# Performance work log

Measured on AMD Instinct MI355X. Metric: run time of the kernel, lower is better.

The kernel has to match this reference:

```python
import jax, jax.numpy as jnp
import numpy as np

N, IN_DIM, OUT_DIM = 8192, 512, 512
ALPHA = 0.2  # leaky relu negative slope
NEG_BIG = -9e15

def _xavier(key, shape, gain=1.414):
    fan_in, fan_out = shape[0], shape[1]
    bound = gain * np.sqrt(6.0 / (fan_in + fan_out))
    return jax.random.uniform(key, shape, jnp.float32, -bound, bound)

def setup_inputs() -> dict:
    key = jax.random.key(0)
    k1, k2, k3, k4 = jax.random.split(key, 4)
    h = jax.random.normal(k1, (N, IN_DIM), jnp.float32)
    adj = jax.random.randint(k2, (N, N), 0, 2, jnp.int32)
    W = _xavier(k3, (IN_DIM, OUT_DIM))
    a = _xavier(k4, (2 * OUT_DIM, 1))
    return {"h": h, "adj": adj, "W": W, "a": a}

def reference(h, adj, W, a):
    Wh = h @ W                              # [N, out]
    # e_ij = leakyrelu(a1 . Wh_i + a2 . Wh_j) without the O(N^2*2d) concat
    a1 = a[:OUT_DIM, 0]                     # [out]
    a2 = a[OUT_DIM:, 0]                     # [out]
    f1 = Wh @ a1                            # [N]
    f2 = Wh @ a2                            # [N]
    e = jax.nn.leaky_relu(f1[:, None] + f2[None, :], negative_slope=ALPHA)
    e = jnp.where(adj > 0, e, NEG_BIG)
    attention = jax.nn.softmax(e, axis=1)   # dropout is identity in eval mode
    h_prime = attention @ Wh                # [N, out]
    return jax.nn.elu(h_prime)              # concat=True branch
```

## Files before the change

### kernel.cpp

```cpp
#include <hip/hip_runtime.h>
#include <stdint.h>

#define NN   8192
#define DIN  512
#define DOUT 512
#define ALPHA 0.2f

typedef float          floatx4  __attribute__((ext_vector_type(4)));
typedef float          floatx2  __attribute__((ext_vector_type(2)));
typedef short          shortx8  __attribute__((ext_vector_type(8)));
typedef unsigned short ushortx4 __attribute__((ext_vector_type(4)));
typedef int            intx2    __attribute__((ext_vector_type(2)));
typedef int            intx4    __attribute__((ext_vector_type(4)));
typedef unsigned       uintx2   __attribute__((ext_vector_type(2)));

__device__ inline unsigned short f2bf(float x) {
    union { float f; unsigned u; } v; v.f = x;
    return (unsigned short)((v.u + 0x7FFFu + ((v.u >> 16) & 1u)) >> 16);
}
__device__ inline unsigned encf(float x) {
    union { float f; unsigned u; } v; v.f = x;
    return (v.u & 0x80000000u) ? ~v.u : (v.u | 0x80000000u);
}
__device__ inline float decf(unsigned e) {
    union { float f; unsigned u; } v;
    v.u = (e & 0x80000000u) ? (e & 0x7FFFFFFFu) : ~e;
    return v.f;
}
__device__ inline float lrelu(float x) { return fmaxf(x, ALPHA * x); }

__global__ __launch_bounds__(256) void transpose_w(const float* __restrict__ W,
                                                   unsigned short* __restrict__ WT) {
    __shared__ float tile[32][33];
    const int t = threadIdx.x;
    const int x = t & 31, y = t >> 5;
    const int tr = (blockIdx.x >> 4) * 32, tc = (blockIdx.x & 15) * 32;
#pragma unroll
    for (int i = 0; i < 4; i++) {
        int r = y + i * 8;
        tile[r][x] = W[(size_t)(tr + r) * DOUT + tc + x];
    }
    __syncthreads();
#pragma unroll
    for (int i = 0; i < 4; i++) {
        int r = y + i * 8;
        WT[(size_t)(tc + r) * DIN + tr + x] = f2bf(tile[x][r]);
    }
}

__global__ __launch_bounds__(256) void gemm_wh(
    const float* __restrict__ h, const unsigned short* __restrict__ WT,
    const float* __restrict__ a, unsigned short* __restrict__ WhTt,
    float* __restrict__ f1, float* __restrict__ f2, unsigned* __restrict__ Menc)
{
    __shared__ float f1s[4][16], f2s[4][16];
    const int t = threadIdx.x;
    const int w = t >> 6, lane = t & 63, l15 = lane & 15, q = lane >> 4;
    const int r0 = blockIdx.x * 16;
    const int wc0 = w * 128;

    floatx4 acc[8];
    const floatx4 z4 = {0.f, 0.f, 0.f, 0.f};
#pragma unroll
    for (int j = 0; j < 8; j++) acc[j] = z4;

    const float* hp = &h[(size_t)(r0 + l15) * DIN + q * 8];
    const unsigned short* bp = &WT[(size_t)(wc0 + l15) * DIN + q * 8];

    floatx4 hA[2][2];
    shortx8 bB[2][8];
    hA[0][0] = *(const floatx4*)hp;
    hA[0][1] = *(const floatx4*)(hp + 4);
#pragma unroll
    for (int nt = 0; nt < 8; nt++)
        bB[0][nt] = *(const shortx8*)(bp + (size_t)nt * 16 * DIN);

#pragma unroll 2
    for (int it = 0; it < 16; ++it) {
        const int c = it & 1, n = c ^ 1;
        const int kn = ((it + 1) & 15) * 32;
        hA[n][0] = *(const floatx4*)(hp + kn);
        hA[n][1] = *(const floatx4*)(hp + kn + 4);
#pragma unroll
        for (int nt = 0; nt < 8; nt++)
            bB[n][nt] = *(const shortx8*)(bp + (size_t)nt * 16 * DIN + kn);

        shortx8 af;
#pragma unroll
        for (int j = 0; j < 8; j++)
            af[j] = (short)f2bf(hA[c][j >> 2][j & 3]);
#pragma unroll
        for (int nt = 0; nt < 8; nt++)
            acc[nt] = __builtin_amdgcn_mfma_f32_16x16x32_bf16(af, bB[c][nt], acc[nt], 0, 0, 0);
    }

    float a1v[8], a2v[8];
#pragma unroll
    for (int nt = 0; nt < 8; nt++) {
        int col = wc0 + nt * 16 + l15;
        a1v[nt] = a[col];
        a2v[nt] = a[DOUT + col];
    }
    {
        const int kk0 = r0 + q * 4;
        const int tile_k = kk0 >> 5;
        const int qq = (kk0 >> 3) & 3;
        const int j0 = kk0 & 7;
#pragma unroll
        for (int nt = 0; nt < 8; nt++) {
            const int tile_n = w * 8 + nt;
            ushortx4 pk;
#pragma unroll
            for (int reg = 0; reg < 4; reg++) pk[reg] = f2bf(acc[nt][reg]);
            *(ushortx4*)&WhTt[(((size_t)tile_k * 32 + tile_n) << 9) + qq * 128 + l15 * 8 + j0] = pk;
        }
    }
    float s1a[4], s2a[4];
#pragma unroll
    for (int reg = 0; reg < 4; reg++) {
        float s1 = 0.f, s2 = 0.f;
#pragma unroll
        for (int nt = 0; nt < 8; nt++) {
            s1 += acc[nt][reg] * a1v[nt];
            s2 += acc[nt][reg] * a2v[nt];
        }
        s1 += __shfl_xor(s1, 1, 64); s2 += __shfl_xor(s2, 1, 64);
        s1 += __shfl_xor(s1, 2, 64); s2 += __shfl_xor(s2, 2, 64);
        s1 += __shfl_xor(s1, 4, 64); s2 += __shfl_xor(s2, 4, 64);
        s1 += __shfl_xor(s1, 8, 64); s2 += __shfl_xor(s2, 8, 64);
        s1a[reg] = s1; s2a[reg] = s2;
    }
    if (l15 == 0) {
#pragma unroll
        for (int reg = 0; reg < 4; reg++) {
            f1s[w][q * 4 + reg] = s1a[reg];
            f2s[w][q * 4 + reg] = s2a[reg];
        }
    }
    __syncthreads();
    if (t < 16) {
        float v1 = f1s[0][t] + f1s[1][t] + f1s[2][t] + f1s[3][t];
        float v2 = f2s[0][t] + f2s[1][t] + f2s[2][t] + f2s[3][t];
        f1[r0 + t] = v1;
        f2[r0 + t] = v2;
        float mx = v2;
        mx = fmaxf(mx, __shfl_xor(mx, 1, 64));
        mx = fmaxf(mx, __shfl_xor(mx, 2, 64));
        mx = fmaxf(mx, __shfl_xor(mx, 4, 64));
        mx = fmaxf(mx, __shfl_xor(mx, 8, 64));
        if (t == 0) atomicMax(Menc, encf(mx));
    }
}

__global__ __launch_bounds__(1024, 4) void gat_agg(
    const int* __restrict__ adj, const unsigned short* __restrict__ WhTt,
    const float* __restrict__ f1, const float* __restrict__ f2,
    const unsigned* __restrict__ Menc, float* __restrict__ P,
    float* __restrict__ D)
{
    __shared__ __align__(16) unsigned short pbuf[2][4][128 * 40];
    __shared__ float f2s[2048];
    __shared__ float lsp[8][128];

    const int t = threadIdx.x;
    const int w = t >> 6, lane = t & 63, l15 = lane & 15, q = lane >> 4;
    const int prow = t >> 3, pk = t & 7;

    const int kq = blockIdx.x & 3;
    const int rgid = blockIdx.x >> 2;
    const int r0 = rgid * 128;
    const int k0 = kq * 2048;
    const int it0 = ((blockIdx.x >> 3) * 4) & 63;

    *(floatx2*)&f2s[t * 2] = *(const floatx2*)&f2[k0 + t * 2];

    const float M = decf(*Menc);
    const float f1v = f1[r0 + prow];
    const float mi = lrelu(f1v + M);

    floatx4 acc[8][2];
    const floatx4 z4 = {0.f, 0.f, 0.f, 0.f};
#pragma unroll
    for (int i = 0; i < 8; i++)
#pragma unroll
        for (int j = 0; j < 2; j++) acc[i][j] = z4;
    float ls = 0.f;

    const unsigned short* bpp = WhTt
        + (((size_t)(kq * 64) * 32 + w * 2) << 9) + lane * 8;
    const int* arp = adj + (size_t)(r0 + prow) * NN + k0 + pk * 4;

    intx4   adjr[4];
    shortx8 breg[2][2];

    __syncthreads();

#pragma unroll
    for (int j = 0; j < 4; j++)
        adjr[j] = __builtin_nontemporal_load((const intx4*)(arp + ((it0 + j) & 63) * 32));
    breg[0][0] = *(const shortx8*)(bpp + (size_t)it0 * 16384);
    breg[0][1] = *(const shortx8*)(bpp + (size_t)it0 * 16384 + 512);

#pragma unroll 1
    for (int g = 0; g < 16; ++g) {
        const int gb = g & 1;

#pragma unroll
        for (int j = 0; j < 4; j++) {
            const int px = (g * 4 + j + it0) & 63;
            const floatx4 ff = *(const floatx4*)&f2s[px * 32 + pk * 4];
            const intx4   ad = adjr[j];
            float p0 = __expf(lrelu(f1v + ff[0]) - mi);
            float p1 = __expf(lrelu(f1v + ff[1]) - mi);
            float p2 = __expf(lrelu(f1v + ff[2]) - mi);
            float p3 = __expf(lrelu(f1v + ff[3]) - mi);
            p0 = (ad[0] > 0) ? p0 : 0.f;
            p1 = (ad[1] > 0) ? p1 : 0.f;
            p2 = (ad[2] > 0) ? p2 : 0.f;
            p3 = (ad[3] > 0) ? p3 : 0.f;
            ls += (p0 + p1) + (p2 + p3);
            uintx2 dd;
            dd[0] = __builtin_amdgcn_perm(__float_as_uint(p1), __float_as_uint(p0), 0x07060302u);
            dd[1] = __builtin_amdgcn_perm(__float_as_uint(p3), __float_as_uint(p2), 0x07060302u);
            *(uintx2*)&pbuf[gb][j][prow * 40 + pk * 4] = dd;
        }

        {
            const int gn = (g + 1) & 15;
#pragma unroll
            for (int j = 0; j < 4; j++)
                adjr[j] = __builtin_nontemporal_load(
                    (const intx4*)(arp + ((gn * 4 + j + it0) & 63) * 32));
        }

        asm volatile("s_waitcnt lgkmcnt(0)" ::: "memory");
        __builtin_amdgcn_s_barrier();

#pragma unroll
        for (int j = 0; j < 4; j++) {
            const int c = (g * 4 + j) & 1, n = c ^ 1;
            const int pxn = (g * 4 + j + 1 + it0) & 63;
            breg[n][0] = *(const shortx8*)(bpp + (size_t)pxn * 16384);
            breg[n][1] = *(const shortx8*)(bpp + (size_t)pxn * 16384 + 512);

            __builtin_amdgcn_s_setprio(1);
#pragma unroll
            for (int rg = 0; rg < 8; rg++) {
                const shortx8 af = *(const shortx8*)&pbuf[gb][j][(rg * 16 + l15) * 40 + q * 8];
                acc[rg][0] = __builtin_amdgcn_mfma_f32_16x16x32_bf16(af, breg[c][0], acc[rg][0], 0, 0, 0);
                acc[rg][1] = __builtin_amdgcn_mfma_f32_16x16x32_bf16(af, breg[c][1], acc[rg][1], 0, 0, 0);
            }
            __builtin_amdgcn_s_setprio(0);
        }
    }

    __syncthreads();
    lsp[pk][prow] = ls;
    __syncthreads();
    if (t < 128) {
        float s = 0.f;
#pragma unroll
        for (int kc = 0; kc < 8; kc++) s += lsp[kc][t];
        D[kq * NN + r0 + t] = s;
    }

    float* Pq = P + (size_t)kq * ((size_t)NN * DOUT) + (size_t)r0 * DOUT;
#pragma unroll
    for (int rg = 0; rg < 8; rg++)
#pragma unroll
        for (int nt = 0; nt < 2; nt++) {
            const int col = w * 32 + nt * 16 + l15;
#pragma unroll
            for (int reg = 0; reg < 4; reg++) {
                const int row = rg * 16 + q * 4 + reg;
                Pq[(size_t)row * DOUT + col] = acc[rg][nt][reg];
            }
        }
}

__global__ __launch_bounds__(1024) void gat_fin(
    const float* __restrict__ P, const float* __restrict__ D,
    float* __restrict__ out)
{
    const int t = threadIdx.x;
    const int r0 = blockIdx.x * 32;
    const int rr = t >> 7;
    const int c4 = (t & 127) * 4;
    const size_t Q = (size_t)NN * DOUT;
#pragma unroll
    for (int j = 0; j < 4; j++) {
        const int row = r0 + j * 8 + rr;
        const float den = ((D[row] + D[NN + row]) + (D[2 * NN + row] + D[3 * NN + row]));
        const float li = 1.f / den;
        const size_t off = (size_t)row * DOUT + c4;
        floatx4 v0 = *(const floatx4*)(P + off);
        floatx4 v1 = *(const floatx4*)(P + Q + off);
        floatx4 v2 = *(const floatx4*)(P + 2 * Q + off);
        floatx4 v3 = *(const floatx4*)(P + 3 * Q + off);
        floatx4 s;
#pragma unroll
        for (int i = 0; i < 4; i++) {
            float x = ((v0[i] + v1[i]) + (v2[i] + v3[i])) * li;
            s[i] = (x > 0.f) ? x : (__expf(x) - 1.f);
        }
        __builtin_nontemporal_store(s, (floatx4*)(out + off));
    }
}

extern "C" void kernel_launch(void* const* d_in, const int* in_sizes, int n_in,
                              void* d_out, int out_size, void* d_ws, size_t ws_size,
                              hipStream_t stream) {
    const float* h   = (const float*)d_in[0];
    const int*   adj = (const int*)d_in[1];
    const float* W   = (const float*)d_in[2];
    const float* a   = (const float*)d_in[3];
    float* out = (float*)d_out;

    char* ws = (char*)d_ws;
    unsigned short* WT    = (unsigned short*)ws;
    unsigned short* WhTt  = (unsigned short*)(ws + 524288);
    float*          f1    = (float*)(ws + 8912896);
    float*          f2    = (float*)(ws + 8945664);
    unsigned*       Menc  = (unsigned*)(ws + 8978432);
    float*          D     = (float*)(ws + 9437184);
    float*          P     = (float*)(ws + 16777216);

    hipMemsetAsync(Menc, 0, 4, stream);
    transpose_w<<<256, 256, 0, stream>>>(W, WT);
    gemm_wh<<<512, 256, 0, stream>>>(h, WT, a, WhTt, f1, f2, Menc);
    gat_agg<<<256, 1024, 0, stream>>>(adj, WhTt, f1, f2, Menc, P, D);
    gat_fin<<<256, 1024, 0, stream>>>(P, D, out);
}
```

Measured before the change: 432.8 us.

## Software-pipeline softmax P-tile computation with MFMA over double-buffered LDS

Restructures the aggregation loop so the exp/mask computation for the next group of tiles is interleaved with the MFMA work on the current group, writing into the other LDS buffer. A prologue fills the first buffer, and there is now one barrier per group, after the MFMAs, instead of one between the two phases. The f2 staging array in shared memory is removed and f2 is read straight from global memory (likely cache hits). The intent is to hide exp and adjacency-load latency behind matrix-core work. The cost is higher register pressure and more global loads of f2.

```diff
diff --git a/kernel.cpp b/kernel.cpp
--- a/kernel.cpp
+++ b/kernel.cpp
@@ -159,7 +159,6 @@
     float* __restrict__ D)
 {
     __shared__ __align__(16) unsigned short pbuf[2][4][128 * 40];
-    __shared__ float f2s[2048];
     __shared__ float lsp[8][128];
 
     const int t = threadIdx.x;
@@ -172,8 +171,6 @@
     const int k0 = kq * 2048;
     const int it0 = ((blockIdx.x >> 3) * 4) & 63;
 
-    *(floatx2*)&f2s[t * 2] = *(const floatx2*)&f2[k0 + t * 2];
-
     const float M = decf(*Menc);
     const float f1v = f1[r0 + prow];
     const float mi = lrelu(f1v + M);
@@ -189,59 +186,74 @@
     const unsigned short* bpp = WhTt
         + (((size_t)(kq * 64) * 32 + w * 2) << 9) + lane * 8;
     const int* arp = adj + (size_t)(r0 + prow) * NN + k0 + pk * 4;
+    const float* fpq = f2 + k0 + pk * 4;
 
     intx4   adjr[4];
     shortx8 breg[2][2];
 
-    __syncthreads();
-
 #pragma unroll
     for (int j = 0; j < 4; j++)
         adjr[j] = __builtin_nontemporal_load((const intx4*)(arp + ((it0 + j) & 63) * 32));
+#pragma unroll
+    for (int j = 0; j < 4; j++) {
+        const int px = (it0 + j) & 63;
+        const floatx4 ff = *(const floatx4*)(fpq + px * 32);
+        const intx4   ad = adjr[j];
+        float p0 = __expf(lrelu(f1v + ff[0]) - mi);
+        float p1 = __expf(lrelu(f1v + ff[1]) - mi);
+        float p2 = __expf(lrelu(f1v + ff[2]) - mi);
+        float p3 = __expf(lrelu(f1v + ff[3]) - mi);
+        p0 = (ad[0] > 0) ? p0 : 0.f;
+        p1 = (ad[1] > 0) ? p1 : 0.f;
+        p2 = (ad[2] > 0) ? p2 : 0.f;
+        p3 = (ad[3] > 0) ? p3 : 0.f;
+        ls += (p0 + p1) + (p2 + p3);
+        uintx2 dd;
+        dd[0] = __builtin_amdgcn_perm(__float_as_uint(p1), __float_as_uint(p0), 0x07060302u);
+        dd[1] = __builtin_amdgcn_perm(__float_as_uint(p3), __float_as_uint(p2), 0x07060302u);
+        *(uintx2*)&pbuf[0][j][prow * 40 + pk * 4] = dd;
+    }
+#pragma unroll
+    for (int j = 0; j < 4; j++)
+        adjr[j] = __builtin_nontemporal_load((const intx4*)(arp + ((4 + j + it0) & 63) * 32));
     breg[0][0] = *(const shortx8*)(bpp + (size_t)it0 * 16384);
     breg[0][1] = *(const shortx8*)(bpp + (size_t)it0 * 16384 + 512);
+    asm volatile("s_waitcnt lgkmcnt(0)" ::: "memory");
+    __builtin_amdgcn_s_barrier();
 
 #pragma unroll 1
     for (int g = 0; g < 16; ++g) {
         const int gb = g & 1;
-
 #pragma unroll
         for (int j = 0; j < 4; j++) {
-            const int px = (g * 4 + j + it0) & 63;
-            const floatx4 ff = *(const floatx4*)&f2s[px * 32 + pk * 4];
-            const intx4   ad = adjr[j];
-            float p0 = __expf(lrelu(f1v + ff[0]) - mi);
-            float p1 = __expf(lrelu(f1v + ff[1]) - mi);
-            float p2 = __expf(lrelu(f1v + ff[2]) - mi);
-            float p3 = __expf(lrelu(f1v + ff[3]) - mi);
-            p0 = (ad[0] > 0) ? p0 : 0.f;
-            p1 = (ad[1] > 0) ? p1 : 0.f;
-            p2 = (ad[2] > 0) ? p2 : 0.f;
-            p3 = (ad[3] > 0) ? p3 : 0.f;
-            ls += (p0 + p1) + (p2 + p3);
-            uintx2 dd;
-            dd[0] = __builtin_amdgcn_perm(__float_as_uint(p1), __float_as_uint(p0), 0x07060302u);
-            dd[1] = __builtin_amdgcn_perm(__float_as_uint(p3), __float_as_uint(p2), 0x07060302u);
-            *(uintx2*)&pbuf[gb][j][prow * 40 + pk * 4] = dd;
-        }
-
-        {
-            const int gn = (g + 1) & 15;
-#pragma unroll
-            for (int j = 0; j < 4; j++)
-                adjr[j] = __builtin_nontemporal_load(
-                    (const intx4*)(arp + ((gn * 4 + j + it0) & 63) * 32));
-        }
-
-        asm volatile("s_waitcnt lgkmcnt(0)" ::: "memory");
-        __builtin_amdgcn_s_barrier();
-
-#pragma unroll
-        for (int j = 0; j < 4; j++) {
-            const int c = (g * 4 + j) & 1, n = c ^ 1;
-            const int pxn = (g * 4 + j + 1 + it0) & 63;
+            const int ft = g * 4 + j;
+            const int c = ft & 1, n = c ^ 1;
+            const int pxn = (ft + 1 + it0) & 63;
+
             breg[n][0] = *(const shortx8*)(bpp + (size_t)pxn * 16384);
             breg[n][1] = *(const shortx8*)(bpp + (size_t)pxn * 16384 + 512);
+
+            if (g < 15) {
+                const int px = ((g + 1) * 4 + j + it0) & 63;
+                const floatx4 ff = *(const floatx4*)(fpq + px * 32);
+                const intx4   ad = adjr[j];
+                float p0 = __expf(lrelu(f1v + ff[0]) - mi);
+                float p1 = __expf(lrelu(f1v + ff[1]) - mi);
+                float p2 = __expf(lrelu(f1v + ff[2]) - mi);
+                float p3 = __expf(lrelu(f1v + ff[3]) - mi);
+                p0 = (ad[0] > 0) ? p0 : 0.f;
+                p1 = (ad[1] > 0) ? p1 : 0.f;
+                p2 = (ad[2] > 0) ? p2 : 0.f;
+                p3 = (ad[3] > 0) ? p3 : 0.f;
+                ls += (p0 + p1) + (p2 + p3);
+                uintx2 dd;
+                dd[0] = __builtin_amdgcn_perm(__float_as_uint(p1), __float_as_uint(p0), 0x07060302u);
+                dd[1] = __builtin_amdgcn_perm(__float_as_uint(p3), __float_as_uint(p2), 0x07060302u);
+                *(uintx2*)&pbuf[gb ^ 1][j][prow * 40 + pk * 4] = dd;
+                if (g < 14)
+                    adjr[j] = __builtin_nontemporal_load(
+                        (const intx4*)(arp + (((g + 2) * 4 + j + it0) & 63) * 32));
+            }
 
             __builtin_amdgcn_s_setprio(1);
 #pragma unroll
@@ -252,6 +264,8 @@
             }
             __builtin_amdgcn_s_setprio(0);
         }
+        asm volatile("s_waitcnt lgkmcnt(0)" ::: "memory");
+        __builtin_amdgcn_s_barrier();
     }
 
     __syncthreads();
```

After: 500.3 us. 15.6% more time.

## Store partial accumulators in fragment-native layout and remap in finalize kernel

Applied to the files above, without the earlier changes.

The attention kernel now writes each MFMA accumulator fragment as one contiguous 16-byte vector store in a fragment-ordered layout, replacing scattered strided scalar stores. The finalize kernel reads the four partials in that same layout with coalesced vector loads, takes per-row inverse denominators from shared memory, and does the layout-to-row-major transposition while storing the output. The aim is to make the large partial-sum writes coalesced. In exchange, the final output stores become scalar and partly strided.

```diff
diff --git a/kernel.cpp b/kernel.cpp
--- a/kernel.cpp
+++ b/kernel.cpp
@@ -264,46 +264,54 @@
         D[kq * NN + r0 + t] = s;
     }
 
-    float* Pq = P + (size_t)kq * ((size_t)NN * DOUT) + (size_t)r0 * DOUT;
+    float* Pq = P + (size_t)kq * ((size_t)NN * DOUT)
+                  + (size_t)rgid * 65536 + w * 4096;
 #pragma unroll
     for (int rg = 0; rg < 8; rg++)
 #pragma unroll
-        for (int nt = 0; nt < 2; nt++) {
-            const int col = w * 32 + nt * 16 + l15;
-#pragma unroll
-            for (int reg = 0; reg < 4; reg++) {
-                const int row = rg * 16 + q * 4 + reg;
-                Pq[(size_t)row * DOUT + col] = acc[rg][nt][reg];
-            }
-        }
+        for (int nt = 0; nt < 2; nt++)
+            *(floatx4*)&Pq[(rg * 2 + nt) * 256 + lane * 4] = acc[rg][nt];
 }
 
 __global__ __launch_bounds__(1024) void gat_fin(
     const float* __restrict__ P, const float* __restrict__ D,
     float* __restrict__ out)
 {
+    __shared__ float linv[128];
     const int t = threadIdx.x;
-    const int r0 = blockIdx.x * 32;
-    const int rr = t >> 7;
-    const int c4 = (t & 127) * 4;
+    const int rgid = blockIdx.x >> 2, wq = blockIdx.x & 3;
+    const int r0 = rgid * 128;
+
+    if (t < 128) {
+        const int row = r0 + t;
+        const float den = (D[row] + D[NN + row]) + (D[2 * NN + row] + D[3 * NN + row]);
+        linv[t] = 1.f / den;
+    }
+    __syncthreads();
+
+    const int v = t >> 6, lane = t & 63, l15 = lane & 15, q = lane >> 4;
+    const int w = wq * 4 + (v & 3);
+    const int fg = v >> 2;
     const size_t Q = (size_t)NN * DOUT;
-#pragma unroll
-    for (int j = 0; j < 4; j++) {
-        const int row = r0 + j * 8 + rr;
-        const float den = ((D[row] + D[NN + row]) + (D[2 * NN + row] + D[3 * NN + row]));
-        const float li = 1.f / den;
-        const size_t off = (size_t)row * DOUT + c4;
-        floatx4 v0 = *(const floatx4*)(P + off);
-        floatx4 v1 = *(const floatx4*)(P + Q + off);
-        floatx4 v2 = *(const floatx4*)(P + 2 * Q + off);
-        floatx4 v3 = *(const floatx4*)(P + 3 * Q + off);
-        floatx4 s;
-#pragma unroll
-        for (int i = 0; i < 4; i++) {
-            float x = ((v0[i] + v1[i]) + (v2[i] + v3[i])) * li;
-            s[i] = (x > 0.f) ? x : (__expf(x) - 1.f);
-        }
-        __builtin_nontemporal_store(s, (floatx4*)(out + off));
+    const size_t base = (size_t)rgid * 65536 + w * 4096;
+
+#pragma unroll
+    for (int f = 0; f < 4; f++) {
+        const int fr = fg * 4 + f;
+        const int rg = fr >> 1, nt = fr & 1;
+        const size_t off = base + fr * 256 + lane * 4;
+        const floatx4 v0 = *(const floatx4*)(P + off);
+        const floatx4 v1 = *(const floatx4*)(P + Q + off);
+        const floatx4 v2 = *(const floatx4*)(P + 2 * Q + off);
+        const floatx4 v3 = *(const floatx4*)(P + 3 * Q + off);
+        const int row0 = rg * 16 + q * 4;
+        const int col = w * 32 + nt * 16 + l15;
+#pragma unroll
+        for (int reg = 0; reg < 4; reg++) {
+            float x = ((v0[reg] + v1[reg]) + (v2[reg] + v3[reg])) * linv[row0 + reg];
+            x = (x > 0.f) ? x : (__expf(x) - 1.f);
+            __builtin_nontemporal_store(x, out + (size_t)(r0 + row0 + reg) * DOUT + col);
+        }
     }
 }
 
```

Result: no change. 439.7 us (+1.6%).
